# Kernel optimization log

Hardware: AMD Instinct MI355X
Metric: run time of the kernel (lower is better)

The kernel has to match this reference:

```python
import jax, jax.numpy as jnp
import numpy as np

N_IN = 100000   # active voxels at coarse level
N_OUT = 400000  # active voxels at fine level
K = 8           # 2x2x2 kernel offsets of the inverse conv
P = 100000      # rulebook pairs per kernel offset
C_IN, C_OUT, C_SKIP = 128, 64, 64
EPS = 1e-5


def setup_inputs() -> dict:
    key = jax.random.key(0)
    k1, k2, k3, k4, k5, k6 = jax.random.split(key, 6)
    x_feats = jax.random.normal(k1, (N_IN, C_IN), jnp.float32)
    skip_feats = jax.random.normal(k2, (N_OUT, C_SKIP), jnp.float32)
    W_deconv = jax.random.normal(k3, (K, C_IN, C_OUT), jnp.float32) * (1.0 / np.sqrt(C_IN * K))
    gamma = jnp.ones((C_OUT,), jnp.float32)
    beta = jnp.zeros((C_OUT,), jnp.float32)
    W_fuse = jax.random.normal(k4, (C_OUT + C_SKIP, C_OUT), jnp.float32) * (1.0 / np.sqrt(C_OUT + C_SKIP))
    in_idx = jax.random.randint(k5, (K, P), 0, N_IN, jnp.int32)
    out_idx = jax.random.randint(k6, (K, P), 0, N_OUT, jnp.int32)
    return {"x_feats": x_feats, "skip_feats": skip_feats, "W_deconv": W_deconv,
            "gamma": gamma, "beta": beta, "W_fuse": W_fuse,
            "in_idx": in_idx, "out_idx": out_idx}


def reference(x_feats, skip_feats, W_deconv, gamma, beta, W_fuse, in_idx, out_idx):
    # --- SparseInverseConv3d: gather-GEMM-scatter over the rulebook ---
    gathered = x_feats[in_idx]                                  # [K,P,C_IN]
    contrib = jnp.einsum('kpi,kio->kpo', gathered, W_deconv)    # [K,P,C_OUT]
    y = jnp.zeros((N_OUT, C_OUT), x_feats.dtype)
    y = y.at[out_idx.reshape(-1)].add(contrib.reshape(-1, C_OUT))
    # --- BatchNorm1d (batch stats, biased var) + ReLU on voxel features ---
    mean = jnp.mean(y, axis=0)
    var = jnp.mean((y - mean) ** 2, axis=0)
    y = (y - mean) * jax.lax.rsqrt(var + EPS) * gamma + beta
    y = jax.nn.relu(y)
    # --- channel concat with skip, then SubMConv3d(kernel=1) == linear ---
    z = jnp.concatenate([y, skip_feats], axis=1)                # [N_OUT, C_OUT+C_SKIP]
    return z @ W_fuse                                           # [N_OUT, C_OUT]
```

## Files before the change

### kernel.cpp

```cpp
#include <hip/hip_runtime.h>

#define N_IN   100000
#define N_OUT  400000
#define KK     8
#define PP     100000
#define C_IN   128
#define C_OUTC 64
#define C_SKIP 64
#define EPS_BN 1e-5f
#define SLOTS  16

typedef __attribute__((ext_vector_type(8))) short bf16x8;
typedef __attribute__((ext_vector_type(4))) float f32x4;

__device__ __forceinline__ unsigned short f2b(float f) {
    unsigned int u = __builtin_bit_cast(unsigned int, f);
    return (unsigned short)((u + 0x7FFFu + ((u >> 16) & 1u)) >> 16);
}
__device__ __forceinline__ float b2f(unsigned short v) {
    return __builtin_bit_cast(float, (unsigned)v << 16);
}

__global__ __launch_bounds__(256) void prep_all(
    const float* __restrict__ Wd, unsigned short* __restrict__ bfrag,
    int4* __restrict__ counts4, float4* __restrict__ mid4)
{
    const int t = blockIdx.x * 256 + threadIdx.x;
    if (t < N_OUT / 4)
        counts4[t] = (int4){0, 0, 0, 0};
    if (t < (32 * 128) / 4)
        mid4[t] = (float4){0.f, 0.f, 0.f, 0.f};
    if (t < KK * 4 * 4 * 64 * 8) {
        const int j  = t & 7;
        const int l  = (t >> 3) & 63;
        const int ct = (t >> 9) & 3;
        const int ks = (t >> 11) & 3;
        const int ko = t >> 13;
        const int i  = ks * 32 + (l >> 4) * 8 + j;
        const int c  = ct * 16 + (l & 15);
        bfrag[t] = f2b(Wd[((size_t)ko * C_IN + i) * C_OUTC + c]);
    }
}

__global__ __launch_bounds__(256) void fill_csr(
    const int* __restrict__ in_idx, const int* __restrict__ out_idx,
    int* __restrict__ counts, int* __restrict__ slots)
{
    const int q = blockIdx.x * 256 + threadIdx.x;
    if (q < KK * PP) {
        const int row = out_idx[q];
        const int pk  = in_idx[q] * KK + q / PP;
        const int idx = atomicAdd(&counts[row], 1);
        if (idx < SLOTS) slots[(size_t)row * SLOTS + idx] = pk;
    }
}

__global__ __launch_bounds__(256) void gemm_all(
    const float* __restrict__ x, const unsigned short* __restrict__ bfrag,
    unsigned short* __restrict__ z)
{
    __shared__ __align__(16) unsigned short alds[32 * 136];
    const int rb = blockIdx.x * 32;
    const float4* __restrict__ x4 = (const float4*)(x + (size_t)rb * C_IN);
    for (int e = threadIdx.x; e < 32 * 32; e += 256) {
        const int row = e >> 5, q = e & 31;
        const float4 v = x4[row * 32 + q];
        uint2 p;
        p.x = f2b(v.x) | ((unsigned)f2b(v.y) << 16);
        p.y = f2b(v.z) | ((unsigned)f2b(v.w) << 16);
        *(uint2*)(&alds[row * 136 + q * 4]) = p;
    }
    __syncthreads();

    const int wv  = threadIdx.x >> 6;
    const int l   = threadIdx.x & 63;
    const int r16 = l & 15, hi = l >> 4;

    f32x4 acc[2][2][4];
    #pragma unroll
    for (int q = 0; q < 2; ++q)
        #pragma unroll
        for (int rt = 0; rt < 2; ++rt)
            #pragma unroll
            for (int ct = 0; ct < 4; ++ct)
                acc[q][rt][ct] = (f32x4){0.f, 0.f, 0.f, 0.f};

    #pragma unroll
    for (int ks = 0; ks < 4; ++ks) {
        const bf16x8 a0 = *(const bf16x8*)(&alds[r16 * 136 + ks * 32 + hi * 8]);
        const bf16x8 a1 = *(const bf16x8*)(&alds[(16 + r16) * 136 + ks * 32 + hi * 8]);
        #pragma unroll
        for (int q = 0; q < 2; ++q) {
            const unsigned short* __restrict__ bk = bfrag + (size_t)(wv * 2 + q) * 8192;
            #pragma unroll
            for (int ct = 0; ct < 4; ++ct) {
                const bf16x8 b = *(const bf16x8*)(bk + ((ks * 4 + ct) * 64 + l) * 8);
                acc[q][0][ct] = __builtin_amdgcn_mfma_f32_16x16x32_bf16(a0, b, acc[q][0][ct], 0, 0, 0);
                acc[q][1][ct] = __builtin_amdgcn_mfma_f32_16x16x32_bf16(a1, b, acc[q][1][ct], 0, 0, 0);
            }
        }
    }

    #pragma unroll
    for (int q = 0; q < 2; ++q) {
        const int k = wv * 2 + q;
        #pragma unroll
        for (int rt = 0; rt < 2; ++rt)
            #pragma unroll
            for (int ct = 0; ct < 4; ++ct)
                #pragma unroll
                for (int j = 0; j < 4; ++j)
                    z[((size_t)(rb + rt * 16 + hi * 4 + j) * KK + k) * 64 + ct * 16 + r16]
                        = f2b(acc[q][rt][ct][j]);
    }
}

__global__ __launch_bounds__(512) void gather_yb(
    const unsigned short* __restrict__ z, const int* __restrict__ counts,
    const int* __restrict__ slots, unsigned short* __restrict__ yb,
    float* __restrict__ mid)
{
    const int tid = threadIdx.x, lane = tid & 63;
    const int gw  = (int)blockIdx.x * 8 + (tid >> 6);
    const int r0  = gw * 8;

    const int4 c0 = *(const int4*)(counts + r0);
    const int4 c1 = *(const int4*)(counts + r0 + 4);
    const int cnt[8] = {c0.x, c0.y, c0.z, c0.w, c1.x, c1.y, c1.z, c1.w};
    int4 s4[8];
    #pragma unroll
    for (int i = 0; i < 8; ++i)
        s4[i] = *(const int4*)(slots + (size_t)(r0 + i) * SLOTS);

    float ssum = 0.f, ssq = 0.f;
    float a[8];
    #pragma unroll
    for (int i = 0; i < 8; ++i) {
        const int c  = cnt[i] > SLOTS ? SLOTS : cnt[i];
        const int p0 = c > 0 ? s4[i].x : 0;
        const int p1 = c > 1 ? s4[i].y : 0;
        const int p2 = c > 2 ? s4[i].z : 0;
        const int p3 = c > 3 ? s4[i].w : 0;
        const float v0 = b2f(z[(size_t)p0 * 64 + lane]);
        const float v1 = b2f(z[(size_t)p1 * 64 + lane]);
        const float v2 = b2f(z[(size_t)p2 * 64 + lane]);
        const float v3 = b2f(z[(size_t)p3 * 64 + lane]);
        float s = (c > 0 ? v0 : 0.f) + (c > 1 ? v1 : 0.f);
        s += (c > 2 ? v2 : 0.f) + (c > 3 ? v3 : 0.f);
        if (c > 4) {
            for (int j = 4; j < c; ++j)
                s += b2f(z[(size_t)slots[(size_t)(r0 + i) * SLOTS + j] * 64 + lane]);
        }
        a[i] = s;
    }
    #pragma unroll
    for (int i = 0; i < 8; ++i) {
        yb[(size_t)(r0 + i) * C_OUTC + lane] = f2b(a[i]);
        ssum += a[i];
        ssq = fmaf(a[i], a[i], ssq);
    }

    __shared__ float rs[512], rq[512];
    rs[tid] = ssum; rq[tid] = ssq;
    __syncthreads();
    if (tid < 64) {
        float s = 0.f, q2 = 0.f;
        #pragma unroll
        for (int w = 0; w < 8; ++w) { s += rs[tid + w * 64]; q2 += rq[tid + w * 64]; }
        float* mrow = mid + (size_t)(blockIdx.x & 31) * 128;
        atomicAdd(&mrow[tid], s);
        atomicAdd(&mrow[64 + tid], q2);
    }
}

__global__ void finalize_p(const float* __restrict__ mid,
                           const float* __restrict__ gamma,
                           const float* __restrict__ beta,
                           const float* __restrict__ Wf,
                           float* __restrict__ sc,
                           unsigned short* __restrict__ wf_frag)
{
    __shared__ float acc2[128];
    __shared__ float bsh[C_OUTC];
    __shared__ float ssc[C_OUTC];
    const int t = threadIdx.x;
    float s = 0.f;
    #pragma unroll
    for (int b = 0; b < 32; ++b) s += mid[(size_t)b * 128 + t];
    acc2[t] = s;
    __syncthreads();
    if (t < 64) {
        const float inv_n = 1.0f / (float)N_OUT;
        const float mean  = acc2[t] * inv_n;
        const float var   = acc2[64 + t] * inv_n - mean * mean;
        const float sg    = gamma[t] * rsqrtf(var + EPS_BN);
        const float b     = beta[t] - mean * sg;
        sc[t]            = sg;
        sc[C_OUTC + t]   = -b / sg;
        ssc[t] = sg;
        bsh[t] = b;
    }
    __syncthreads();
    if (t < 64) {
        float acc = 0.f;
        for (int i = 0; i < C_OUTC; ++i)
            acc = fmaf(bsh[i], Wf[i * C_OUTC + t], acc);
        sc[2 * C_OUTC + t] = acc;
    }
    for (int e = t; e < 4 * 4 * 64 * 8; e += 128) {
        const int j  = e & 7;
        const int l  = (e >> 3) & 63;
        const int ct = (e >> 9) & 3;
        const int ks = e >> 11;
        const int i  = ks * 32 + (l >> 4) * 8 + j;
        const int c  = ct * 16 + (l & 15);
        float w = Wf[(size_t)i * C_OUTC + c];
        if (i < C_OUTC) w *= ssc[i];
        wf_frag[e] = f2b(w);
    }
}

__global__ __launch_bounds__(256) void fuse_mfma_b(
    const unsigned short* __restrict__ yb, const float* __restrict__ skip,
    const unsigned short* __restrict__ wf_frag, const float* __restrict__ sc,
    float* __restrict__ out)
{
    __shared__ __align__(16) unsigned short alds[128 * 136];
    __shared__ float nbsh[C_OUTC];
    const int rb = blockIdx.x * 128;
    if (threadIdx.x < C_OUTC) nbsh[threadIdx.x] = sc[C_OUTC + threadIdx.x];
    __syncthreads();

    const uint4* __restrict__ yb4 = (const uint4*)(yb + (size_t)rb * C_OUTC);
    for (int e = threadIdx.x; e < 128 * 8; e += 256) {
        const int row = e >> 3, q = e & 7;
        uint4 v = yb4[row * 8 + q];
        uint4 o;
        unsigned* vp = (unsigned*)&v;
        unsigned* op = (unsigned*)&o;
        #pragma unroll
        for (int h = 0; h < 4; ++h) {
            const float lo = fmaxf(b2f((unsigned short)(vp[h] & 0xFFFF)), nbsh[q * 8 + h * 2]);
            const float hf = fmaxf(b2f((unsigned short)(vp[h] >> 16)),    nbsh[q * 8 + h * 2 + 1]);
            op[h] = f2b(lo) | ((unsigned)f2b(hf) << 16);
        }
        *(uint4*)(&alds[row * 136 + q * 8]) = o;
    }
    const float4* __restrict__ s4 = (const float4*)(skip + (size_t)rb * C_SKIP);
    for (int e = threadIdx.x; e < 128 * 16; e += 256) {
        const int row = e >> 4, q = e & 15;
        const float4 v = s4[row * 16 + q];
        uint2 p;
        p.x = f2b(v.x) | ((unsigned)f2b(v.y) << 16);
        p.y = f2b(v.z) | ((unsigned)f2b(v.w) << 16);
        *(uint2*)(&alds[row * 136 + 64 + q * 4]) = p;
    }
    __syncthreads();

    const int w   = threadIdx.x >> 6;
    const int l   = threadIdx.x & 63;
    const int r16 = l & 15, hi = l >> 4;
    const int rw  = w * 32;

    f32x4 acc[2][4];
    #pragma unroll
    for (int ct = 0; ct < 4; ++ct) {
        const float b0 = sc[2 * C_OUTC + ct * 16 + r16];
        acc[0][ct] = (f32x4){b0, b0, b0, b0};
        acc[1][ct] = (f32x4){b0, b0, b0, b0};
    }

    #pragma unroll
    for (int ks = 0; ks < 4; ++ks) {
        const bf16x8 a0 = *(const bf16x8*)(&alds[(rw + r16) * 136 + ks * 32 + hi * 8]);
        const bf16x8 a1 = *(const bf16x8*)(&alds[(rw + 16 + r16) * 136 + ks * 32 + hi * 8]);
        #pragma unroll
        for (int ct = 0; ct < 4; ++ct) {
            const bf16x8 b = *(const bf16x8*)(wf_frag + ((ks * 4 + ct) * 64 + l) * 8);
            acc[0][ct] = __builtin_amdgcn_mfma_f32_16x16x32_bf16(a0, b, acc[0][ct], 0, 0, 0);
            acc[1][ct] = __builtin_amdgcn_mfma_f32_16x16x32_bf16(a1, b, acc[1][ct], 0, 0, 0);
        }
    }

    #pragma unroll
    for (int rt = 0; rt < 2; ++rt)
        #pragma unroll
        for (int ct = 0; ct < 4; ++ct)
            #pragma unroll
            for (int j = 0; j < 4; ++j)
                out[(size_t)(rb + rw + rt * 16 + hi * 4 + j) * C_OUTC + ct * 16 + r16]
                    = acc[rt][ct][j];
}

extern "C" void kernel_launch(void* const* d_in, const int* in_sizes, int n_in,
                              void* d_out, int out_size, void* d_ws, size_t ws_size,
                              hipStream_t stream)
{
    const float* x      = (const float*)d_in[0];
    const float* skip   = (const float*)d_in[1];
    const float* Wd     = (const float*)d_in[2];
    const float* gamma  = (const float*)d_in[3];
    const float* beta   = (const float*)d_in[4];
    const float* Wf     = (const float*)d_in[5];
    const int*   in_idx  = (const int*)d_in[6];
    const int*   out_idx = (const int*)d_in[7];

    float* y  = (float*)d_out;
    float* sc = (float*)d_ws + 128;

    char* p = (char*)d_ws + 4096;
    unsigned short* bfrag   = (unsigned short*)p;  p += (size_t)KK * 8192 * 2;
    unsigned short* wf_frag = (unsigned short*)p;  p += 8192 * 2;
    int*   counts   = (int*)p;                     p += (size_t)N_OUT * 4;
    int*   slots    = (int*)p;                     p += (size_t)N_OUT * SLOTS * 4;
    float* mid      = (float*)p;                   p += (size_t)32 * 128 * 4;
    unsigned short* z = (unsigned short*)p;        p += (size_t)N_IN * KK * C_OUTC * 2;
    unsigned short* yb = (unsigned short*)p;

    prep_all<<<(N_OUT / 4 + 255) / 256, 256, 0, stream>>>(
        Wd, bfrag, (int4*)counts, (float4*)mid);
    fill_csr<<<(KK * PP + 255) / 256, 256, 0, stream>>>(in_idx, out_idx, counts, slots);
    gemm_all<<<N_IN / 32, 256, 0, stream>>>(x, bfrag, z);
    gather_yb<<<N_OUT / 64, 512, 0, stream>>>(z, counts, slots, yb, mid);
    finalize_p<<<1, 128, 0, stream>>>(mid, gamma, beta, Wf, sc, wf_frag);
    fuse_mfma_b<<<N_OUT / 128, 256, 0, stream>>>(yb, skip, wf_frag, sc, y);
}
```

Before: 269.3 us.

## Make gemm_all persistent with double-buffered LDS prefetch of x tiles

The dense gemm kernel now runs a fixed grid of 1024 blocks that loop over 32-row tiles of x. Each block loads the next tile into registers while running MFMAs on the current one, then writes it into the other LDS buffer. The aim is to hide global load latency behind compute and to amortize launch and per-block setup. In exchange it uses twice the LDS and more registers, which could reduce occupancy, and the tile count of 3125 does not divide evenly over 1024 blocks, leaving some blocks with an extra tile.

```diff
diff --git a/kernel.cpp b/kernel.cpp
--- a/kernel.cpp
+++ b/kernel.cpp
@@ -9,6 +9,7 @@
 #define C_SKIP 64
 #define EPS_BN 1e-5f
 #define SLOTS  16
+#define GEMM_GRID 1024
 
 typedef __attribute__((ext_vector_type(8))) short bf16x8;
 typedef __attribute__((ext_vector_type(4))) float f32x4;
@@ -59,59 +60,93 @@
     const float* __restrict__ x, const unsigned short* __restrict__ bfrag,
     unsigned short* __restrict__ z)
 {
-    __shared__ __align__(16) unsigned short alds[32 * 136];
-    const int rb = blockIdx.x * 32;
-    const float4* __restrict__ x4 = (const float4*)(x + (size_t)rb * C_IN);
-    for (int e = threadIdx.x; e < 32 * 32; e += 256) {
-        const int row = e >> 5, q = e & 31;
-        const float4 v = x4[row * 32 + q];
+    __shared__ __align__(16) unsigned short lds[2][32 * 136];
+    const int tid = threadIdx.x;
+    const int wv  = tid >> 6;
+    const int l   = tid & 63;
+    const int r16 = l & 15, hi = l >> 4;
+    const int ntiles = N_IN / 32;
+
+    int t = blockIdx.x;
+    float4 ld[4];
+    {
+        const float4* __restrict__ xt = (const float4*)(x + (size_t)t * 32 * C_IN);
+        #pragma unroll
+        for (int i = 0; i < 4; ++i) ld[i] = xt[i * 256 + tid];
+    }
+    #pragma unroll
+    for (int i = 0; i < 4; ++i) {
+        const int e = i * 256 + tid, row = e >> 5, q = e & 31;
         uint2 p;
-        p.x = f2b(v.x) | ((unsigned)f2b(v.y) << 16);
-        p.y = f2b(v.z) | ((unsigned)f2b(v.w) << 16);
-        *(uint2*)(&alds[row * 136 + q * 4]) = p;
-    }
-    __syncthreads();
-
-    const int wv  = threadIdx.x >> 6;
-    const int l   = threadIdx.x & 63;
-    const int r16 = l & 15, hi = l >> 4;
-
-    f32x4 acc[2][2][4];
-    #pragma unroll
-    for (int q = 0; q < 2; ++q)
-        #pragma unroll
-        for (int rt = 0; rt < 2; ++rt)
-            #pragma unroll
-            for (int ct = 0; ct < 4; ++ct)
-                acc[q][rt][ct] = (f32x4){0.f, 0.f, 0.f, 0.f};
-
-    #pragma unroll
-    for (int ks = 0; ks < 4; ++ks) {
-        const bf16x8 a0 = *(const bf16x8*)(&alds[r16 * 136 + ks * 32 + hi * 8]);
-        const bf16x8 a1 = *(const bf16x8*)(&alds[(16 + r16) * 136 + ks * 32 + hi * 8]);
+        p.x = f2b(ld[i].x) | ((unsigned)f2b(ld[i].y) << 16);
+        p.y = f2b(ld[i].z) | ((unsigned)f2b(ld[i].w) << 16);
+        *(uint2*)(&lds[0][row * 136 + q * 4]) = p;
+    }
+    __syncthreads();
+    int cur = 0;
+
+    while (true) {
+        const int tn = t + GEMM_GRID;
+        const bool more = tn < ntiles;
+        if (more) {
+            const float4* __restrict__ xt = (const float4*)(x + (size_t)tn * 32 * C_IN);
+            #pragma unroll
+            for (int i = 0; i < 4; ++i) ld[i] = xt[i * 256 + tid];
+        }
+
+        const unsigned short* __restrict__ al = lds[cur];
+        f32x4 acc[2][2][4];
+        #pragma unroll
+        for (int q = 0; q < 2; ++q)
+            #pragma unroll
+            for (int rt = 0; rt < 2; ++rt)
+                #pragma unroll
+                for (int ct = 0; ct < 4; ++ct)
+                    acc[q][rt][ct] = (f32x4){0.f, 0.f, 0.f, 0.f};
+
+        #pragma unroll
+        for (int ks = 0; ks < 4; ++ks) {
+            const bf16x8 a0 = *(const bf16x8*)(&al[r16 * 136 + ks * 32 + hi * 8]);
+            const bf16x8 a1 = *(const bf16x8*)(&al[(16 + r16) * 136 + ks * 32 + hi * 8]);
+            #pragma unroll
+            for (int q = 0; q < 2; ++q) {
+                const unsigned short* __restrict__ bk = bfrag + (size_t)(wv * 2 + q) * 8192;
+                #pragma unroll
+                for (int ct = 0; ct < 4; ++ct) {
+                    const bf16x8 b = *(const bf16x8*)(bk + ((ks * 4 + ct) * 64 + l) * 8);
+                    acc[q][0][ct] = __builtin_amdgcn_mfma_f32_16x16x32_bf16(a0, b, acc[q][0][ct], 0, 0, 0);
+                    acc[q][1][ct] = __builtin_amdgcn_mfma_f32_16x16x32_bf16(a1, b, acc[q][1][ct], 0, 0, 0);
+                }
+            }
+        }
+
+        const int rb = t * 32;
         #pragma unroll
         for (int q = 0; q < 2; ++q) {
-            const unsigned short* __restrict__ bk = bfrag + (size_t)(wv * 2 + q) * 8192;
-            #pragma unroll
-            for (int ct = 0; ct < 4; ++ct) {
-                const bf16x8 b = *(const bf16x8*)(bk + ((ks * 4 + ct) * 64 + l) * 8);
-                acc[q][0][ct] = __builtin_amdgcn_mfma_f32_16x16x32_bf16(a0, b, acc[q][0][ct], 0, 0, 0);
-                acc[q][1][ct] = __builtin_amdgcn_mfma_f32_16x16x32_bf16(a1, b, acc[q][1][ct], 0, 0, 0);
-            }
-        }
-    }
-
-    #pragma unroll
-    for (int q = 0; q < 2; ++q) {
-        const int k = wv * 2 + q;
-        #pragma unroll
-        for (int rt = 0; rt < 2; ++rt)
-            #pragma unroll
-            for (int ct = 0; ct < 4; ++ct)
+            const int k = wv * 2 + q;
+            #pragma unroll
+            for (int rt = 0; rt < 2; ++rt)
                 #pragma unroll
-                for (int j = 0; j < 4; ++j)
-                    z[((size_t)(rb + rt * 16 + hi * 4 + j) * KK + k) * 64 + ct * 16 + r16]
-                        = f2b(acc[q][rt][ct][j]);
+                for (int ct = 0; ct < 4; ++ct)
+                    #pragma unroll
+                    for (int j = 0; j < 4; ++j)
+                        z[((size_t)(rb + rt * 16 + hi * 4 + j) * KK + k) * 64 + ct * 16 + r16]
+                            = f2b(acc[q][rt][ct][j]);
+        }
+
+        if (!more) break;
+
+        #pragma unroll
+        for (int i = 0; i < 4; ++i) {
+            const int e = i * 256 + tid, row = e >> 5, q = e & 31;
+            uint2 p;
+            p.x = f2b(ld[i].x) | ((unsigned)f2b(ld[i].y) << 16);
+            p.y = f2b(ld[i].z) | ((unsigned)f2b(ld[i].w) << 16);
+            *(uint2*)(&lds[cur ^ 1][row * 136 + q * 4]) = p;
+        }
+        __syncthreads();
+        cur ^= 1;
+        t = tn;
     }
 }
 
@@ -320,7 +355,7 @@
     prep_all<<<(N_OUT / 4 + 255) / 256, 256, 0, stream>>>(
         Wd, bfrag, (int4*)counts, (float4*)mid);
     fill_csr<<<(KK * PP + 255) / 256, 256, 0, stream>>>(in_idx, out_idx, counts, slots);
-    gemm_all<<<N_IN / 32, 256, 0, stream>>>(x, bfrag, z);
+    gemm_all<<<GEMM_GRID, 256, 0, stream>>>(x, bfrag, z);
     gather_yb<<<N_OUT / 64, 512, 0, stream>>>(z, counts, slots, yb, mid);
     finalize_p<<<1, 128, 0, stream>>>(mid, gamma, beta, Wf, sc, wf_frag);
     fuse_mfma_b<<<N_OUT / 128, 256, 0, stream>>>(yb, skip, wf_frag, sc, y);
```

Result: faster. 244.8 us (-9.1%).
